# Performance work log

Hardware: AMD Instinct MI355X
Metric: run time of the kernel (lower is better)

Reference implementation:

```python
import jax, jax.numpy as jnp
import numpy as np

N_NODES = 100000
N_EDGES = 1600000
D_IN = 128
D_OUT = 128


def setup_inputs() -> dict:
    key = jax.random.key(0)
    k1, k2, k3, k4, k5, k6 = jax.random.split(key, 6)
    x = jax.random.normal(k1, (N_NODES, D_IN), dtype=jnp.float32)
    rows = jax.random.randint(k2, (N_EDGES,), 0, N_NODES, dtype=jnp.int32)
    cols = jax.random.randint(k3, (N_EDGES,), 0, N_NODES, dtype=jnp.int32)
    vals = jax.random.uniform(k4, (N_EDGES,), dtype=jnp.float32)
    # nn.Linear init: U(-1/sqrt(in), 1/sqrt(in))
    bound = 1.0 / np.sqrt(D_IN)
    W = jax.random.uniform(k5, (D_IN, D_OUT), minval=-bound, maxval=bound, dtype=jnp.float32)
    b = jax.random.uniform(k6, (D_OUT,), minval=-bound, maxval=bound, dtype=jnp.float32)
    return {"x": x, "rows": rows, "cols": cols, "vals": vals, "W": W, "b": b}


def reference(x, rows, cols, vals, W, b):
    # support = fc1(x)  -> [N, D_OUT]
    support = x @ W + b
    # output = adj @ support, adj in COO form (rows, cols, vals)
    msg = support[cols] * vals[:, None]          # [E, D_OUT] gather + scale
    out = jax.ops.segment_sum(msg, rows, num_segments=N_NODES)  # scatter-add
    return out
```

## Files before the change

### kernel.cpp

```cpp
#include <hip/hip_runtime.h>

#define D 128
#define NB_MAX 1024
#define CH 4096
#define CAP 2560
#define SP 136

typedef short short8 __attribute__((ext_vector_type(8)));
typedef float floatx4 __attribute__((ext_vector_type(4)));

__device__ inline unsigned short f2bf(float f) {
  unsigned u = __float_as_uint(f);
  u += 0x7fffu + ((u >> 16) & 1u);
  return (unsigned short)(u >> 16);
}

__global__ __launch_bounds__(256) void prep_kernel(
    const float* __restrict__ W, unsigned short* __restrict__ wf,
    const float* __restrict__ x, unsigned short* __restrict__ xh,
    int total_elems, int ncast,
    const int* __restrict__ rows, int* __restrict__ bucket_cnt, int n_edges) {
  __shared__ int h[NB_MAX];
  const int bid = blockIdx.x;
  const int t = threadIdx.x;

  if (bid < 8) {
    int tid = bid * 256 + t;
    int ks = tid >> 9;
    int rem = tid & 511;
    int nt = rem >> 6;
    int lane = rem & 63;
    int n = nt * 16 + (lane & 15);
    int k0 = ks * 32 + (lane >> 4) * 8;
    unsigned short v[8];
#pragma unroll
    for (int j = 0; j < 8; ++j) v[j] = f2bf(W[(k0 + j) * D + n]);
    uint4 o;
    o.x = (unsigned)v[0] | ((unsigned)v[1] << 16);
    o.y = (unsigned)v[2] | ((unsigned)v[3] << 16);
    o.z = (unsigned)v[4] | ((unsigned)v[5] << 16);
    o.w = (unsigned)v[6] | ((unsigned)v[7] << 16);
    ((uint4*)wf)[tid] = o;
    return;
  }

  if (bid < 8 + ncast) {
    int idx = (bid - 8) * 256 + t;
    if (idx * 16 < total_elems) {
      const float4* x4 = (const float4*)x;
      uint4* xh4 = (uint4*)xh;
#pragma unroll
      for (int j = 0; j < 2; ++j) {
        float4 a = x4[idx * 4 + 2 * j];
        float4 c = x4[idx * 4 + 2 * j + 1];
        uint4 o;
        o.x = (unsigned)f2bf(a.x) | ((unsigned)f2bf(a.y) << 16);
        o.y = (unsigned)f2bf(a.z) | ((unsigned)f2bf(a.w) << 16);
        o.z = (unsigned)f2bf(c.x) | ((unsigned)f2bf(c.y) << 16);
        o.w = (unsigned)f2bf(c.z) | ((unsigned)f2bf(c.w) << 16);
        xh4[idx * 2 + j] = o;
      }
    }
    return;
  }

  for (int i = t; i < NB_MAX; i += 256) h[i] = 0;
  __syncthreads();
  int blk = bid - 8 - ncast;
  int lo = blk * 4096;
  int hi = min(lo + 4096, n_edges);
  for (int i = lo + t; i < hi; i += 256) atomicAdd(&h[rows[i] >> 7], 1);
  __syncthreads();
  for (int i = t; i < NB_MAX; i += 256)
    if (h[i]) atomicAdd(&bucket_cnt[i], h[i]);
}

__global__ __launch_bounds__(1024) void bucket_scan_kernel(
    const int* __restrict__ bucket_cnt, int* __restrict__ bucket_off,
    int* __restrict__ bucket_cursor, int nb) {
  __shared__ int s[1024];
  int t = threadIdx.x;
  s[t] = (t < nb) ? bucket_cnt[t] : 0;
  __syncthreads();
  for (int d = 1; d < 1024; d <<= 1) {
    int v = (t >= d) ? s[t - d] : 0;
    __syncthreads();
    s[t] += v;
    __syncthreads();
  }
  int excl = (t == 0) ? 0 : s[t - 1];
  if (t < nb) { bucket_off[t] = excl; bucket_cursor[t] = excl; }
  if (t == nb) bucket_off[t] = s[nb - 1];
}

__global__ __launch_bounds__(256) void partition_kernel(
    const int* __restrict__ rows, const int* __restrict__ cols,
    const float* __restrict__ vals, int* __restrict__ bucket_cursor,
    int2* __restrict__ tmp, int n_edges, int cap) {
  __shared__ int h[NB_MAX];
  __shared__ int base_s[NB_MAX];
  int t = threadIdx.x;
  for (int i = t; i < NB_MAX; i += 256) h[i] = 0;
  __syncthreads();
  int lo = blockIdx.x * CH;
  int hi = min(lo + CH, n_edges);
  for (int i = lo + t; i < hi; i += 256) atomicAdd(&h[rows[i] >> 7], 1);
  __syncthreads();
  for (int i = t; i < NB_MAX; i += 256) {
    int c = h[i];
    base_s[i] = c ? (cap * i + atomicAdd(&bucket_cursor[i], c)) : 0;
    h[i] = 0;
  }
  __syncthreads();
  for (int i = lo + t; i < hi; i += 256) {
    int r = rows[i];
    int bkt = r >> 7;
    int l = atomicAdd(&h[bkt], 1);
    int pos = base_s[bkt] + l;
    if (!cap || pos < (bkt + 1) * cap)
      tmp[pos] = make_int2(((r & 127) << 17) | cols[i], __float_as_int(vals[i]));
  }
}

__global__ __launch_bounds__(1024, 8) void gather_gemm_kernel(
    const uint2* __restrict__ xh, const unsigned short* __restrict__ wf,
    const float* __restrict__ bias, const int* __restrict__ bucket_off,
    const int* __restrict__ bucket_cursor, const int2* __restrict__ tmp,
    float* __restrict__ out, int n_nodes, int cap) {
  __shared__ __align__(16) char U[67584];
  __shared__ int cnt[128];
  __shared__ int scn[128];
  __shared__ int rs[129];
  __shared__ float rowsum[128];
  unsigned short* ys = (unsigned short*)U;
  int2* ebuf = (int2*)U;
  int2* sbuf = (int2*)(U + 34816);
  unsigned short* wfs = (unsigned short*)(U + 34816);
  const int t = threadIdx.x;
  const int b = blockIdx.x;

  const uint4* wf4 = (const uint4*)wf;
  uint4 wfr0 = wf4[t];
  uint4 wfr1 = wf4[t + 1024];

  int lo, ne;
  if (cap) { lo = b * cap; ne = min(bucket_cursor[b], cap); }
  else     { lo = bucket_off[b]; ne = bucket_off[b + 1] - lo; }
  const int slot = t >> 5;
  const int lane = t & 31;

  if (ne <= CAP) {
    if (t < 128) cnt[t] = 0;
    __syncthreads();
    for (int i = t; i < ne; i += 1024) {
      int2 p = tmp[lo + i];
      ebuf[i] = p;
      atomicAdd(&cnt[((unsigned)p.x) >> 17], 1);
    }
    __syncthreads();
    if (t < 128) scn[t] = cnt[t];
    __syncthreads();
#pragma unroll
    for (int d = 1; d < 128; d <<= 1) {
      int v = (t < 128 && t >= d) ? scn[t - d] : 0;
      __syncthreads();
      if (t < 128) scn[t] += v;
      __syncthreads();
    }
    if (t < 128) {
      rs[t] = (t == 0) ? 0 : scn[t - 1];
      cnt[t] = 0;
    }
    __syncthreads();
    if (t == 0) rs[128] = scn[127];
    for (int i = t; i < ne; i += 1024) {
      int2 p = ebuf[i];
      int r = ((unsigned)p.x) >> 17;
      int l = atomicAdd(&cnt[r], 1);
      sbuf[rs[r] + l] = p;
    }
    __syncthreads();
#pragma unroll
    for (int rr = 0; rr < 4; ++rr) {
      int row = slot + (rr << 5);
      int s = rs[row], e = rs[row + 1];
      float4 acc = make_float4(0.f, 0.f, 0.f, 0.f);
      float rsum = 0.f;
      int i = s;
      for (; i + 4 <= e; i += 4) {
        int2 p0 = sbuf[i + 0];
        int2 p1 = sbuf[i + 1];
        int2 p2 = sbuf[i + 2];
        int2 p3 = sbuf[i + 3];
        uint2 s0 = xh[((size_t)(p0.x & 0x1FFFF) << 5) + lane];
        uint2 s1 = xh[((size_t)(p1.x & 0x1FFFF) << 5) + lane];
        uint2 s2 = xh[((size_t)(p2.x & 0x1FFFF) << 5) + lane];
        uint2 s3 = xh[((size_t)(p3.x & 0x1FFFF) << 5) + lane];
        float v0 = __int_as_float(p0.y), v1 = __int_as_float(p1.y);
        float v2 = __int_as_float(p2.y), v3 = __int_as_float(p3.y);
        rsum += v0 + v1 + v2 + v3;
        acc.x += v0 * __uint_as_float(s0.x << 16);
        acc.y += v0 * __uint_as_float(s0.x & 0xffff0000u);
        acc.z += v0 * __uint_as_float(s0.y << 16);
        acc.w += v0 * __uint_as_float(s0.y & 0xffff0000u);
        acc.x += v1 * __uint_as_float(s1.x << 16);
        acc.y += v1 * __uint_as_float(s1.x & 0xffff0000u);
        acc.z += v1 * __uint_as_float(s1.y << 16);
        acc.w += v1 * __uint_as_float(s1.y & 0xffff0000u);
        acc.x += v2 * __uint_as_float(s2.x << 16);
        acc.y += v2 * __uint_as_float(s2.x & 0xffff0000u);
        acc.z += v2 * __uint_as_float(s2.y << 16);
        acc.w += v2 * __uint_as_float(s2.y & 0xffff0000u);
        acc.x += v3 * __uint_as_float(s3.x << 16);
        acc.y += v3 * __uint_as_float(s3.x & 0xffff0000u);
        acc.z += v3 * __uint_as_float(s3.y << 16);
        acc.w += v3 * __uint_as_float(s3.y & 0xffff0000u);
      }
      for (; i < e; ++i) {
        int2 p = sbuf[i];
        float v = __int_as_float(p.y);
        uint2 sv = xh[((size_t)(p.x & 0x1FFFF) << 5) + lane];
        rsum += v;
        acc.x += v * __uint_as_float(sv.x << 16);
        acc.y += v * __uint_as_float(sv.x & 0xffff0000u);
        acc.z += v * __uint_as_float(sv.y << 16);
        acc.w += v * __uint_as_float(sv.y & 0xffff0000u);
      }
      unsigned u0 = (unsigned)f2bf(acc.x) | ((unsigned)f2bf(acc.y) << 16);
      unsigned u1 = (unsigned)f2bf(acc.z) | ((unsigned)f2bf(acc.w) << 16);
      *((uint2*)(ys + row * SP + lane * 4)) = make_uint2(u0, u1);
      if (lane == 0) rowsum[row] = rsum;
    }
  } else {
#pragma unroll
    for (int rr = 0; rr < 4; ++rr) {
      int row = slot + (rr << 5);
      float4 acc = make_float4(0.f, 0.f, 0.f, 0.f);
      float rsum = 0.f;
      for (int i = 0; i < ne; ++i) {
        int2 p = tmp[lo + i];
        if ((int)(((unsigned)p.x) >> 17) != row) continue;
        float v = __int_as_float(p.y);
        uint2 sv = xh[((size_t)(p.x & 0x1FFFF) << 5) + lane];
        rsum += v;
        acc.x += v * __uint_as_float(sv.x << 16);
        acc.y += v * __uint_as_float(sv.x & 0xffff0000u);
        acc.z += v * __uint_as_float(sv.y << 16);
        acc.w += v * __uint_as_float(sv.y & 0xffff0000u);
      }
      unsigned u0 = (unsigned)f2bf(acc.x) | ((unsigned)f2bf(acc.y) << 16);
      unsigned u1 = (unsigned)f2bf(acc.z) | ((unsigned)f2bf(acc.w) << 16);
      *((uint2*)(ys + row * SP + lane * 4)) = make_uint2(u0, u1);
      if (lane == 0) rowsum[row] = rsum;
    }
  }
  __syncthreads();

  uint4* wfs4 = (uint4*)wfs;
  wfs4[t] = wfr0;
  wfs4[t + 1024] = wfr1;
  __syncthreads();

  const int l64 = t & 63;
  const int w = t >> 6;
  const int m = l64 & 15, q = l64 >> 4;
  const int rb = (w & 3) * 32;
  const int cb = (w >> 2) * 32;

  floatx4 acc2[2][2];
#pragma unroll
  for (int rt = 0; rt < 2; ++rt)
#pragma unroll
    for (int ct = 0; ct < 2; ++ct) {
      acc2[rt][ct][0] = 0.f; acc2[rt][ct][1] = 0.f;
      acc2[rt][ct][2] = 0.f; acc2[rt][ct][3] = 0.f;
    }

#pragma unroll
  for (int ks = 0; ks < 4; ++ks) {
    short8 af[2], bfr[2];
#pragma unroll
    for (int rt = 0; rt < 2; ++rt)
      af[rt] = *((const short8*)(ys + (rb + rt * 16 + m) * SP + ks * 32 + q * 8));
#pragma unroll
    for (int ct = 0; ct < 2; ++ct) {
      int nt = (cb >> 4) + ct;
      bfr[ct] = *((const short8*)(wfs + ((ks * 8 + nt) * 64 + l64) * 8));
    }
#pragma unroll
    for (int rt = 0; rt < 2; ++rt)
#pragma unroll
      for (int ct = 0; ct < 2; ++ct)
        acc2[rt][ct] = __builtin_amdgcn_mfma_f32_16x16x32_bf16(
            af[rt], bfr[ct], acc2[rt][ct], 0, 0, 0);
  }

  float b0 = bias[cb + m];
  float b1 = bias[cb + 16 + m];
#pragma unroll
  for (int rt = 0; rt < 2; ++rt)
#pragma unroll
    for (int ct = 0; ct < 2; ++ct) {
      float bc = ct ? b1 : b0;
#pragma unroll
      for (int r = 0; r < 4; ++r) {
        int row = rb + rt * 16 + q * 4 + r;
        int col = cb + ct * 16 + m;
        int node = (b << 7) + row;
        if (node < n_nodes)
          out[(size_t)node * D + col] = acc2[rt][ct][r] + rowsum[row] * bc;
      }
    }
}

extern "C" void kernel_launch(void* const* d_in, const int* in_sizes, int n_in,
                              void* d_out, int out_size, void* d_ws, size_t ws_size,
                              hipStream_t stream) {
  const float* x    = (const float*)d_in[0];
  const int*   rows = (const int*)d_in[1];
  const int*   cols = (const int*)d_in[2];
  const float* vals = (const float*)d_in[3];
  const float* W    = (const float*)d_in[4];
  const float* b    = (const float*)d_in[5];
  float* out = (float*)d_out;

  int n_nodes = in_sizes[0] / D;
  int n_edges = in_sizes[1];
  int nb = (n_nodes + 127) >> 7;
  int total_elems = n_nodes * D;

  size_t xh_bytes = (size_t)total_elems * 2;
  size_t cap_tmp  = (size_t)nb * CAP * 8;
  size_t pk_tmp   = (size_t)n_edges * 8;
  int cap = (ws_size >= xh_bytes + cap_tmp + 45056) ? CAP : 0;
  size_t tmp_sz = cap ? cap_tmp : pk_tmp;

  char* ws = (char*)d_ws;
  unsigned short* xh = (unsigned short*)(ws);
  int2* tmp          = (int2*)(ws + xh_bytes);
  char* mb           = ws + xh_bytes + tmp_sz;
  int* bucket_cnt    = (int*)(mb);
  int* bucket_off    = (int*)(mb + 4096);
  int* bucket_cursor = (int*)(mb + 8192);
  unsigned short* wf = (unsigned short*)(mb + 12288);

  if (cap) hipMemsetAsync(bucket_cursor, 0, NB_MAX * sizeof(int), stream);
  else     hipMemsetAsync(bucket_cnt,    0, NB_MAX * sizeof(int), stream);

  int ncast = (total_elems + 4095) / 4096;
  int ablocks = cap ? 0 : (n_edges + 4095) / 4096;
  prep_kernel<<<dim3(8 + ncast + ablocks), dim3(256), 0, stream>>>(
      W, wf, x, xh, total_elems, ncast, rows, bucket_cnt, n_edges);

  if (!cap)
    bucket_scan_kernel<<<dim3(1), dim3(1024), 0, stream>>>(
        bucket_cnt, bucket_off, bucket_cursor, nb);

  int pblocks = (n_edges + CH - 1) / CH;
  partition_kernel<<<dim3(pblocks), dim3(256), 0, stream>>>(
      rows, cols, vals, bucket_cursor, tmp, n_edges, cap);

  gather_gemm_kernel<<<dim3(nb), dim3(1024), 0, stream>>>(
      (const uint2*)xh, wf, b, bucket_off, bucket_cursor, tmp, out,
      n_nodes, cap);
}
```

Baseline: 231.9 us.

## Replace single-pass edge bucketing with two-level radix partition and packed buckets

Edges are now partitioned in two passes: first into 64 super-buckets of 2048 rows, then each super-bucket is split into 16 buckets of 128 rows. This replaces the single pass that scattered across ~800 buckets into fixed-capacity slots. Fewer scatter destinations per pass should give better write coalescing and less shared-atomic contention. The cost is an extra full read and write of the edge array, plus hardcoded workspace offsets. Because tmp1 aliases xh, the x-to-bf16 cast moves into its own kernel that runs after partitioning.

Measured after the change: 232.9 us. About the same (+0.4%).

```diff
diff --git a/kernel.cpp b/kernel.cpp
--- a/kernel.cpp
+++ b/kernel.cpp
@@ -2,7 +2,8 @@
 
 #define D 128
 #define NB_MAX 1024
-#define CH 4096
+#define NSB_MAX 64
+#define CH1 4096
 #define CAP 2560
 #define SP 136
 
@@ -17,8 +18,6 @@
 
 __global__ __launch_bounds__(256) void prep_kernel(
     const float* __restrict__ W, unsigned short* __restrict__ wf,
-    const float* __restrict__ x, unsigned short* __restrict__ xh,
-    int total_elems, int ncast,
     const int* __restrict__ rows, int* __restrict__ bucket_cnt, int n_edges) {
   __shared__ int h[NB_MAX];
   const int bid = blockIdx.x;
@@ -44,29 +43,9 @@
     return;
   }
 
-  if (bid < 8 + ncast) {
-    int idx = (bid - 8) * 256 + t;
-    if (idx * 16 < total_elems) {
-      const float4* x4 = (const float4*)x;
-      uint4* xh4 = (uint4*)xh;
-#pragma unroll
-      for (int j = 0; j < 2; ++j) {
-        float4 a = x4[idx * 4 + 2 * j];
-        float4 c = x4[idx * 4 + 2 * j + 1];
-        uint4 o;
-        o.x = (unsigned)f2bf(a.x) | ((unsigned)f2bf(a.y) << 16);
-        o.y = (unsigned)f2bf(a.z) | ((unsigned)f2bf(a.w) << 16);
-        o.z = (unsigned)f2bf(c.x) | ((unsigned)f2bf(c.y) << 16);
-        o.w = (unsigned)f2bf(c.z) | ((unsigned)f2bf(c.w) << 16);
-        xh4[idx * 2 + j] = o;
-      }
-    }
-    return;
-  }
-
   for (int i = t; i < NB_MAX; i += 256) h[i] = 0;
   __syncthreads();
-  int blk = bid - 8 - ncast;
+  int blk = bid - 8;
   int lo = blk * 4096;
   int hi = min(lo + 4096, n_edges);
   for (int i = lo + t; i < hi; i += 256) atomicAdd(&h[rows[i] >> 7], 1);
@@ -77,7 +56,8 @@
 
 __global__ __launch_bounds__(1024) void bucket_scan_kernel(
     const int* __restrict__ bucket_cnt, int* __restrict__ bucket_off,
-    int* __restrict__ bucket_cursor, int nb) {
+    int* __restrict__ bucket_cursor, int* __restrict__ sb_off,
+    int* __restrict__ sb_cursor, int nb) {
   __shared__ int s[1024];
   int t = threadIdx.x;
   s[t] = (t < nb) ? bucket_cnt[t] : 0;
@@ -89,44 +69,102 @@
     __syncthreads();
   }
   int excl = (t == 0) ? 0 : s[t - 1];
-  if (t < nb) { bucket_off[t] = excl; bucket_cursor[t] = excl; }
-  if (t == nb) bucket_off[t] = s[nb - 1];
-}
-
-__global__ __launch_bounds__(256) void partition_kernel(
+  if (t < nb) {
+    bucket_off[t] = excl;
+    bucket_cursor[t] = excl;
+    if ((t & 15) == 0) { sb_off[t >> 4] = excl; sb_cursor[t >> 4] = excl; }
+  }
+  if (t == nb) {
+    int total = s[nb - 1];
+    bucket_off[nb] = total;
+    sb_off[(nb + 15) >> 4] = total;
+  }
+}
+
+__global__ __launch_bounds__(256) void sb_partition_kernel(
     const int* __restrict__ rows, const int* __restrict__ cols,
-    const float* __restrict__ vals, int* __restrict__ bucket_cursor,
-    int2* __restrict__ tmp, int n_edges, int cap) {
-  __shared__ int h[NB_MAX];
-  __shared__ int base_s[NB_MAX];
+    const float* __restrict__ vals, int* __restrict__ sb_cursor,
+    int2* __restrict__ tmp1, int n_edges) {
+  __shared__ int h[NSB_MAX];
+  __shared__ int base_s[NSB_MAX];
   int t = threadIdx.x;
-  for (int i = t; i < NB_MAX; i += 256) h[i] = 0;
-  __syncthreads();
-  int lo = blockIdx.x * CH;
-  int hi = min(lo + CH, n_edges);
-  for (int i = lo + t; i < hi; i += 256) atomicAdd(&h[rows[i] >> 7], 1);
-  __syncthreads();
-  for (int i = t; i < NB_MAX; i += 256) {
-    int c = h[i];
-    base_s[i] = c ? (cap * i + atomicAdd(&bucket_cursor[i], c)) : 0;
-    h[i] = 0;
+  if (t < NSB_MAX) h[t] = 0;
+  __syncthreads();
+  int lo = blockIdx.x * CH1;
+  int hi = min(lo + CH1, n_edges);
+  for (int i = lo + t; i < hi; i += 256) atomicAdd(&h[rows[i] >> 11], 1);
+  __syncthreads();
+  if (t < NSB_MAX) {
+    int c = h[t];
+    base_s[t] = c ? atomicAdd(&sb_cursor[t], c) : 0;
+    h[t] = 0;
   }
   __syncthreads();
   for (int i = lo + t; i < hi; i += 256) {
     int r = rows[i];
-    int bkt = r >> 7;
-    int l = atomicAdd(&h[bkt], 1);
-    int pos = base_s[bkt] + l;
-    if (!cap || pos < (bkt + 1) * cap)
-      tmp[pos] = make_int2(((r & 127) << 17) | cols[i], __float_as_int(vals[i]));
+    int s = r >> 11;
+    int l = atomicAdd(&h[s], 1);
+    tmp1[base_s[s] + l] =
+        make_int2(((r & 2047) << 17) | cols[i], __float_as_int(vals[i]));
+  }
+}
+
+__global__ __launch_bounds__(256) void bucket_partition_kernel(
+    const int* __restrict__ sb_off, int* __restrict__ bucket_cursor,
+    const int2* __restrict__ tmp1, int2* __restrict__ tmp2) {
+  __shared__ int h[16];
+  __shared__ int base_s[16];
+  const int s = blockIdx.x >> 4;
+  const int j = blockIdx.x & 15;
+  const int t = threadIdx.x;
+  int lo = sb_off[s], hi = sb_off[s + 1];
+  int n = hi - lo;
+  int sz = (n + 15) >> 4;
+  int a = lo + j * sz;
+  int b = min(a + sz, hi);
+  if (t < 16) h[t] = 0;
+  __syncthreads();
+  for (int i = a + t; i < b; i += 256)
+    atomicAdd(&h[(((unsigned)tmp1[i].x) >> 24) & 15], 1);
+  __syncthreads();
+  if (t < 16) {
+    int c = h[t];
+    base_s[t] = c ? atomicAdd(&bucket_cursor[(s << 4) + t], c) : 0;
+    h[t] = 0;
+  }
+  __syncthreads();
+  for (int i = a + t; i < b; i += 256) {
+    int2 p = tmp1[i];
+    int bi = (((unsigned)p.x) >> 24) & 15;
+    int l = atomicAdd(&h[bi], 1);
+    tmp2[base_s[bi] + l] = make_int2(p.x & 0x00FFFFFF, p.y);
+  }
+}
+
+__global__ __launch_bounds__(256) void xcast_kernel(
+    const float* __restrict__ x, unsigned short* __restrict__ xh,
+    int total_elems) {
+  int idx = blockIdx.x * 256 + threadIdx.x;
+  if (idx * 16 >= total_elems) return;
+  const float4* x4 = (const float4*)x;
+  uint4* xh4 = (uint4*)xh;
+#pragma unroll
+  for (int j = 0; j < 2; ++j) {
+    float4 a = x4[idx * 4 + 2 * j];
+    float4 c = x4[idx * 4 + 2 * j + 1];
+    uint4 o;
+    o.x = (unsigned)f2bf(a.x) | ((unsigned)f2bf(a.y) << 16);
+    o.y = (unsigned)f2bf(a.z) | ((unsigned)f2bf(a.w) << 16);
+    o.z = (unsigned)f2bf(c.x) | ((unsigned)f2bf(c.y) << 16);
+    o.w = (unsigned)f2bf(c.z) | ((unsigned)f2bf(c.w) << 16);
+    xh4[idx * 2 + j] = o;
   }
 }
 
 __global__ __launch_bounds__(1024, 8) void gather_gemm_kernel(
     const uint2* __restrict__ xh, const unsigned short* __restrict__ wf,
     const float* __restrict__ bias, const int* __restrict__ bucket_off,
-    const int* __restrict__ bucket_cursor, const int2* __restrict__ tmp,
-    float* __restrict__ out, int n_nodes, int cap) {
+    const int2* __restrict__ tmp, float* __restrict__ out, int n_nodes) {
   __shared__ __align__(16) char U[67584];
   __shared__ int cnt[128];
   __shared__ int scn[128];
@@ -143,9 +181,8 @@
   uint4 wfr0 = wf4[t];
   uint4 wfr1 = wf4[t + 1024];
 
-  int lo, ne;
-  if (cap) { lo = b * cap; ne = min(bucket_cursor[b], cap); }
-  else     { lo = bucket_off[b]; ne = bucket_off[b + 1] - lo; }
+  const int lo = bucket_off[b];
+  const int ne = bucket_off[b + 1] - lo;
   const int slot = t >> 5;
   const int lane = t & 31;
 
@@ -327,40 +364,40 @@
   int n_nodes = in_sizes[0] / D;
   int n_edges = in_sizes[1];
   int nb = (n_nodes + 127) >> 7;
+  int nsb = (nb + 15) >> 4;
   int total_elems = n_nodes * D;
 
-  size_t xh_bytes = (size_t)total_elems * 2;
-  size_t cap_tmp  = (size_t)nb * CAP * 8;
-  size_t pk_tmp   = (size_t)n_edges * 8;
-  int cap = (ws_size >= xh_bytes + cap_tmp + 45056) ? CAP : 0;
-  size_t tmp_sz = cap ? cap_tmp : pk_tmp;
-
   char* ws = (char*)d_ws;
+  int2* tmp1         = (int2*)(ws);
   unsigned short* xh = (unsigned short*)(ws);
-  int2* tmp          = (int2*)(ws + xh_bytes);
-  char* mb           = ws + xh_bytes + tmp_sz;
+  int2* tmp2         = (int2*)(ws + 25600000);
+  char* mb           = ws + 38400000;
   int* bucket_cnt    = (int*)(mb);
   int* bucket_off    = (int*)(mb + 4096);
   int* bucket_cursor = (int*)(mb + 8192);
-  unsigned short* wf = (unsigned short*)(mb + 12288);
-
-  if (cap) hipMemsetAsync(bucket_cursor, 0, NB_MAX * sizeof(int), stream);
-  else     hipMemsetAsync(bucket_cnt,    0, NB_MAX * sizeof(int), stream);
-
-  int ncast = (total_elems + 4095) / 4096;
-  int ablocks = cap ? 0 : (n_edges + 4095) / 4096;
-  prep_kernel<<<dim3(8 + ncast + ablocks), dim3(256), 0, stream>>>(
-      W, wf, x, xh, total_elems, ncast, rows, bucket_cnt, n_edges);
-
-  if (!cap)
-    bucket_scan_kernel<<<dim3(1), dim3(1024), 0, stream>>>(
-        bucket_cnt, bucket_off, bucket_cursor, nb);
-
-  int pblocks = (n_edges + CH - 1) / CH;
-  partition_kernel<<<dim3(pblocks), dim3(256), 0, stream>>>(
-      rows, cols, vals, bucket_cursor, tmp, n_edges, cap);
+  int* sb_off        = (int*)(mb + 12288);
+  int* sb_cursor     = (int*)(mb + 12800);
+  unsigned short* wf = (unsigned short*)(mb + 13312);
+
+  hipMemsetAsync(bucket_cnt, 0, NB_MAX * sizeof(int), stream);
+
+  int ablocks = (n_edges + 4095) / 4096;
+  prep_kernel<<<dim3(8 + ablocks), dim3(256), 0, stream>>>(
+      W, wf, rows, bucket_cnt, n_edges);
+
+  bucket_scan_kernel<<<dim3(1), dim3(1024), 0, stream>>>(
+      bucket_cnt, bucket_off, bucket_cursor, sb_off, sb_cursor, nb);
+
+  int p1blocks = (n_edges + CH1 - 1) / CH1;
+  sb_partition_kernel<<<dim3(p1blocks), dim3(256), 0, stream>>>(
+      rows, cols, vals, sb_cursor, tmp1, n_edges);
+
+  bucket_partition_kernel<<<dim3(nsb * 16), dim3(256), 0, stream>>>(
+      sb_off, bucket_cursor, tmp1, tmp2);
+
+  int cblocks = (total_elems + 4095) / 4096;
+  xcast_kernel<<<dim3(cblocks), dim3(256), 0, stream>>>(x, xh, total_elems);
 
   gather_gemm_kernel<<<dim3(nb), dim3(1024), 0, stream>>>(
-      (const uint2*)xh, wf, b, bucket_off, bucket_cursor, tmp, out,
-      n_nodes, cap);
-}
+      (const uint2*)xh, wf, b, bucket_off, tmp2, out, n_nodes);
+}
```

## Replace atomic bucket counting with per-chunk histograms and deterministic partition offsets

Applied to the files above, without the earlier changes.

Replaces the capped-bucket scheme (memset, global atomics on bucket cursors, and a fallback scan kernel) with per-chunk row-bucket histograms written to scratch held in the output buffer. The partition kernel then computes bucket offsets and per-chunk prefixes itself, so each edge is written to a packed slot with no global atomics and no memset. This removes a kernel launch and contention on global atomics. In exchange, every partition block reads all chunk histograms, and the workspace offsets are hardcoded to the test sizes.

Result: slower. 283.0 us (+22.0%).

```diff
diff --git a/kernel.cpp b/kernel.cpp
--- a/kernel.cpp
+++ b/kernel.cpp
@@ -2,7 +2,7 @@
 
 #define D 128
 #define NB_MAX 1024
-#define CH 4096
+#define CHN 6250
 #define CAP 2560
 #define SP 136
 
@@ -15,17 +15,28 @@
   return (unsigned short)(u >> 16);
 }
 
-__global__ __launch_bounds__(256) void prep_kernel(
+__global__ __launch_bounds__(1024) void prep_kernel(
     const float* __restrict__ W, unsigned short* __restrict__ wf,
     const float* __restrict__ x, unsigned short* __restrict__ xh,
-    int total_elems, int ncast,
-    const int* __restrict__ rows, int* __restrict__ bucket_cnt, int n_edges) {
+    const int* __restrict__ rows, int* __restrict__ chunk_hist,
+    int n_edges, int nchunks, int nb, int total_elems) {
   __shared__ int h[NB_MAX];
   const int bid = blockIdx.x;
   const int t = threadIdx.x;
 
-  if (bid < 8) {
-    int tid = bid * 256 + t;
+  if (bid < nchunks) {
+    h[t] = 0;
+    __syncthreads();
+    int lo = bid * CHN;
+    int hi = min(lo + CHN, n_edges);
+    for (int i = lo + t; i < hi; i += 1024) atomicAdd(&h[rows[i] >> 7], 1);
+    __syncthreads();
+    if (t < nb) chunk_hist[bid * nb + t] = h[t];
+    return;
+  }
+
+  if (bid < nchunks + 2) {
+    int tid = (bid - nchunks) * 1024 + t;
     int ks = tid >> 9;
     int rem = tid & 511;
     int nt = rem >> 6;
@@ -44,89 +55,75 @@
     return;
   }
 
-  if (bid < 8 + ncast) {
-    int idx = (bid - 8) * 256 + t;
-    if (idx * 16 < total_elems) {
-      const float4* x4 = (const float4*)x;
-      uint4* xh4 = (uint4*)xh;
-#pragma unroll
-      for (int j = 0; j < 2; ++j) {
-        float4 a = x4[idx * 4 + 2 * j];
-        float4 c = x4[idx * 4 + 2 * j + 1];
-        uint4 o;
-        o.x = (unsigned)f2bf(a.x) | ((unsigned)f2bf(a.y) << 16);
-        o.y = (unsigned)f2bf(a.z) | ((unsigned)f2bf(a.w) << 16);
-        o.z = (unsigned)f2bf(c.x) | ((unsigned)f2bf(c.y) << 16);
-        o.w = (unsigned)f2bf(c.z) | ((unsigned)f2bf(c.w) << 16);
-        xh4[idx * 2 + j] = o;
-      }
-    }
-    return;
-  }
-
-  for (int i = t; i < NB_MAX; i += 256) h[i] = 0;
-  __syncthreads();
-  int blk = bid - 8 - ncast;
-  int lo = blk * 4096;
-  int hi = min(lo + 4096, n_edges);
-  for (int i = lo + t; i < hi; i += 256) atomicAdd(&h[rows[i] >> 7], 1);
-  __syncthreads();
-  for (int i = t; i < NB_MAX; i += 256)
-    if (h[i]) atomicAdd(&bucket_cnt[i], h[i]);
-}
-
-__global__ __launch_bounds__(1024) void bucket_scan_kernel(
-    const int* __restrict__ bucket_cnt, int* __restrict__ bucket_off,
-    int* __restrict__ bucket_cursor, int nb) {
-  __shared__ int s[1024];
-  int t = threadIdx.x;
-  s[t] = (t < nb) ? bucket_cnt[t] : 0;
+  int idx = (bid - nchunks - 2) * 1024 + t;
+  if (idx * 16 < total_elems) {
+    const float4* x4 = (const float4*)x;
+    uint4* xh4 = (uint4*)xh;
+#pragma unroll
+    for (int j = 0; j < 2; ++j) {
+      float4 a = x4[idx * 4 + 2 * j];
+      float4 c = x4[idx * 4 + 2 * j + 1];
+      uint4 o;
+      o.x = (unsigned)f2bf(a.x) | ((unsigned)f2bf(a.y) << 16);
+      o.y = (unsigned)f2bf(a.z) | ((unsigned)f2bf(a.w) << 16);
+      o.z = (unsigned)f2bf(c.x) | ((unsigned)f2bf(c.y) << 16);
+      o.w = (unsigned)f2bf(c.z) | ((unsigned)f2bf(c.w) << 16);
+      xh4[idx * 2 + j] = o;
+    }
+  }
+}
+
+__global__ __launch_bounds__(1024) void partition_kernel(
+    const int* __restrict__ rows, const int* __restrict__ cols,
+    const float* __restrict__ vals, const int* __restrict__ chunk_hist,
+    int* __restrict__ bucket_off, int2* __restrict__ tmp,
+    int n_edges, int nchunks, int nb) {
+  __shared__ int pscn[NB_MAX];
+  __shared__ int h[NB_MAX];
+  __shared__ int base_s[NB_MAX];
+  const int c = blockIdx.x;
+  const int t = threadIdx.x;
+
+  int tot = 0, pre = 0;
+  if (t < nb) {
+    for (int cc = 0; cc < nchunks; ++cc) {
+      int v = chunk_hist[cc * nb + t];
+      tot += v;
+      pre += (cc < c) ? v : 0;
+    }
+  }
+  pscn[t] = (t < nb) ? tot : 0;
   __syncthreads();
   for (int d = 1; d < 1024; d <<= 1) {
-    int v = (t >= d) ? s[t - d] : 0;
-    __syncthreads();
-    s[t] += v;
-    __syncthreads();
-  }
-  int excl = (t == 0) ? 0 : s[t - 1];
-  if (t < nb) { bucket_off[t] = excl; bucket_cursor[t] = excl; }
-  if (t == nb) bucket_off[t] = s[nb - 1];
-}
-
-__global__ __launch_bounds__(256) void partition_kernel(
-    const int* __restrict__ rows, const int* __restrict__ cols,
-    const float* __restrict__ vals, int* __restrict__ bucket_cursor,
-    int2* __restrict__ tmp, int n_edges, int cap) {
-  __shared__ int h[NB_MAX];
-  __shared__ int base_s[NB_MAX];
-  int t = threadIdx.x;
-  for (int i = t; i < NB_MAX; i += 256) h[i] = 0;
+    int v = (t >= d) ? pscn[t - d] : 0;
+    __syncthreads();
+    pscn[t] += v;
+    __syncthreads();
+  }
+  int excl = (t == 0) ? 0 : pscn[t - 1];
+  if (c == 0) {
+    if (t < nb) bucket_off[t] = excl;
+    if (t == 0) bucket_off[nb] = pscn[nb - 1];
+  }
+  base_s[t] = excl + pre;
+  h[t] = 0;
   __syncthreads();
-  int lo = blockIdx.x * CH;
-  int hi = min(lo + CH, n_edges);
-  for (int i = lo + t; i < hi; i += 256) atomicAdd(&h[rows[i] >> 7], 1);
-  __syncthreads();
-  for (int i = t; i < NB_MAX; i += 256) {
-    int c = h[i];
-    base_s[i] = c ? (cap * i + atomicAdd(&bucket_cursor[i], c)) : 0;
-    h[i] = 0;
-  }
-  __syncthreads();
-  for (int i = lo + t; i < hi; i += 256) {
+
+  int lo = c * CHN;
+  int hi = min(lo + CHN, n_edges);
+  for (int i = lo + t; i < hi; i += 1024) {
     int r = rows[i];
     int bkt = r >> 7;
     int l = atomicAdd(&h[bkt], 1);
-    int pos = base_s[bkt] + l;
-    if (!cap || pos < (bkt + 1) * cap)
-      tmp[pos] = make_int2(((r & 127) << 17) | cols[i], __float_as_int(vals[i]));
+    tmp[base_s[bkt] + l] =
+        make_int2(((r & 127) << 17) | cols[i], __float_as_int(vals[i]));
   }
 }
 
 __global__ __launch_bounds__(1024, 8) void gather_gemm_kernel(
     const uint2* __restrict__ xh, const unsigned short* __restrict__ wf,
     const float* __restrict__ bias, const int* __restrict__ bucket_off,
-    const int* __restrict__ bucket_cursor, const int2* __restrict__ tmp,
-    float* __restrict__ out, int n_nodes, int cap) {
+    const int2* __restrict__ tmp, float* __restrict__ out, int n_nodes) {
   __shared__ __align__(16) char U[67584];
   __shared__ int cnt[128];
   __shared__ int scn[128];
@@ -143,9 +140,8 @@
   uint4 wfr0 = wf4[t];
   uint4 wfr1 = wf4[t + 1024];
 
-  int lo, ne;
-  if (cap) { lo = b * cap; ne = min(bucket_cursor[b], cap); }
-  else     { lo = bucket_off[b]; ne = bucket_off[b + 1] - lo; }
+  const int lo = bucket_off[b];
+  const int ne = bucket_off[b + 1] - lo;
   const int slot = t >> 5;
   const int lane = t & 31;
 
@@ -327,40 +323,24 @@
   int n_nodes = in_sizes[0] / D;
   int n_edges = in_sizes[1];
   int nb = (n_nodes + 127) >> 7;
+  int nchunks = (n_edges + CHN - 1) / CHN;
   int total_elems = n_nodes * D;
-
-  size_t xh_bytes = (size_t)total_elems * 2;
-  size_t cap_tmp  = (size_t)nb * CAP * 8;
-  size_t pk_tmp   = (size_t)n_edges * 8;
-  int cap = (ws_size >= xh_bytes + cap_tmp + 45056) ? CAP : 0;
-  size_t tmp_sz = cap ? cap_tmp : pk_tmp;
 
   char* ws = (char*)d_ws;
   unsigned short* xh = (unsigned short*)(ws);
-  int2* tmp          = (int2*)(ws + xh_bytes);
-  char* mb           = ws + xh_bytes + tmp_sz;
-  int* bucket_cnt    = (int*)(mb);
-  int* bucket_off    = (int*)(mb + 4096);
-  int* bucket_cursor = (int*)(mb + 8192);
-  unsigned short* wf = (unsigned short*)(mb + 12288);
-
-  if (cap) hipMemsetAsync(bucket_cursor, 0, NB_MAX * sizeof(int), stream);
-  else     hipMemsetAsync(bucket_cnt,    0, NB_MAX * sizeof(int), stream);
-
-  int ncast = (total_elems + 4095) / 4096;
-  int ablocks = cap ? 0 : (n_edges + 4095) / 4096;
-  prep_kernel<<<dim3(8 + ncast + ablocks), dim3(256), 0, stream>>>(
-      W, wf, x, xh, total_elems, ncast, rows, bucket_cnt, n_edges);
-
-  if (!cap)
-    bucket_scan_kernel<<<dim3(1), dim3(1024), 0, stream>>>(
-        bucket_cnt, bucket_off, bucket_cursor, nb);
-
-  int pblocks = (n_edges + CH - 1) / CH;
-  partition_kernel<<<dim3(pblocks), dim3(256), 0, stream>>>(
-      rows, cols, vals, bucket_cursor, tmp, n_edges, cap);
+  int2* tmp          = (int2*)(ws + 25600000);
+  char* mb           = ws + 38400000;
+  int* bucket_off    = (int*)(mb);
+  unsigned short* wf = (unsigned short*)(mb + 4096);
+  int* chunk_hist    = (int*)out;
+
+  int ncast = (total_elems + 16383) / 16384;
+  prep_kernel<<<dim3(nchunks + 2 + ncast), dim3(1024), 0, stream>>>(
+      W, wf, x, xh, rows, chunk_hist, n_edges, nchunks, nb, total_elems);
+
+  partition_kernel<<<dim3(nchunks), dim3(1024), 0, stream>>>(
+      rows, cols, vals, chunk_hist, bucket_off, tmp, n_edges, nchunks, nb);
 
   gather_gemm_kernel<<<dim3(nb), dim3(1024), 0, stream>>>(
-      (const uint2*)xh, wf, b, bucket_off, bucket_cursor, tmp, out,
-      n_nodes, cap);
-}
+      (const uint2*)xh, wf, b, bucket_off, tmp, out, n_nodes);
+}
```
